# Kernel tuning notes

Hardware: AMD Instinct MI355X
Metric: run time of the kernel (lower is better)

The kernel has to match this reference:

```python
import jax, jax.numpy as jnp
import numpy as np

B, T, N, H, P = 16, 64, 512, 128, 12


def _laplacian_with_self_loop(adj):
    a = adj + jnp.eye(adj.shape[0], dtype=adj.dtype)
    d_inv_sqrt = 1.0 / jnp.sqrt(a.sum(axis=1))
    return a * d_inv_sqrt[:, None] * d_inv_sqrt[None, :]


def setup_inputs() -> dict:
    key = jax.random.key(0)
    ks = jax.random.split(key, 10)
    inputs = jax.random.normal(ks[0], (B, T, N), dtype=jnp.float32)
    adj = jax.random.uniform(ks[1], (N, N), dtype=jnp.float32)
    adj = (adj + adj.T) * 0.5
    laplacian = _laplacian_with_self_loop(adj)

    def xavier(k, shape):
        fan_in, fan_out = shape[0], shape[1]
        lim = np.sqrt(6.0 / (fan_in + fan_out))
        return jax.random.uniform(k, shape, jnp.float32, -lim, lim)

    W1 = xavier(ks[2], (H + 1, 2 * H))      # graph_conv1 weights
    b1 = jnp.ones((2 * H,), jnp.float32)    # bias init 1.0
    W2 = xavier(ks[3], (H + 1, H))          # graph_conv2 weights
    b2 = jnp.zeros((H,), jnp.float32)
    att_w1 = xavier(ks[4], (H, 1))
    att_w2 = xavier(ks[5], (N, 1))
    att_w3 = xavier(ks[6], (N, 1))
    att_b1 = jnp.zeros((1,), jnp.float32)
    att_b2 = jnp.zeros((1,), jnp.float32)
    att_b3 = jnp.zeros((1,), jnp.float32)
    W_out = xavier(ks[7], (T, P))
    b_out = jnp.zeros((P,), jnp.float32)
    return dict(inputs=inputs, laplacian=laplacian, W1=W1, b1=b1, W2=W2, b2=b2,
                att_w1=att_w1, att_w2=att_w2, att_w3=att_w3,
                att_b1=att_b1, att_b2=att_b2, att_b3=att_b3,
                W_out=W_out, b_out=b_out)


def reference(inputs, laplacian, W1, b1, W2, b2,
              att_w1, att_w2, att_w3, att_b1, att_b2, att_b3,
              W_out, b_out):
    Bs, Ts, Ns = inputs.shape
    Hs = W2.shape[1]

    def graph_conv(x_t, h_flat, W, b):
        # x_t: [B,N]; h_flat: [B, N*H]
        h = h_flat.reshape(Bs, Ns, Hs)
        conc = jnp.concatenate([x_t[..., None], h], axis=-1)     # [B,N,H+1]
        agg = jnp.einsum('mn,bnc->bmc', laplacian, conc)          # [B,N,H+1]
        out = agg @ W + b                                         # [B,N,O]
        return out.reshape(Bs, -1)                                # [B,N*O] (flattened, matching torch)

    def step(h_flat, x_t):
        ru = jax.nn.sigmoid(graph_conv(x_t, h_flat, W1, b1))      # [B, N*2H]
        r, u = jnp.split(ru, 2, axis=1)                            # split on flattened dim (faithful)
        c = jnp.tanh(graph_conv(x_t, r * h_flat, W2, b2))          # [B, N*H]
        new_h = u * h_flat + (1.0 - u) * c
        return new_h, new_h

    h0 = jnp.zeros((Bs, Ns * Hs), inputs.dtype)
    _, hs = jax.lax.scan(step, h0, jnp.moveaxis(inputs, 1, 0))     # [T,B,N*H]
    hidden_states = jnp.moveaxis(hs, 0, 1).reshape(Bs, Ts, Ns, Hs)

    # SelfAttention: project H->1, then N->1 per (b,t), softmax over T
    hs1 = hidden_states.reshape(-1, Hs) @ att_w1 + att_b1          # [B*T*N, 1]
    f = (hs1.reshape(-1, Ns) @ att_w2 + att_b2).reshape(Bs, Ts)
    g = (hs1.reshape(-1, Ns) @ att_w3 + att_b3).reshape(Bs, Ts)
    beta = jax.nn.softmax(g * f, axis=-1)                          # [B,T]
    context = beta[:, :, None] * hs1.reshape(Bs, Ts, Ns)           # [B,T,N]

    context = context.transpose(0, 2, 1)                           # [B,N,T]
    Ps = W_out.shape[1]
    out = (context.reshape(-1, Ts) @ W_out + b_out).reshape(Bs, Ns, Ps)
    return out.transpose(0, 2, 1)                                  # [B,pre_len,N]
```

## Files before the change

kernel.cpp:

```cpp
#include <hip/hip_runtime.h>
#include <math.h>

#define B_ 16
#define T_ 64
#define N_ 512
#define H_ 128
#define P_ 12
#define NH 65536

__global__ __launch_bounds__(512) void lx_kernel(const float* __restrict__ x,
                                                 const float* __restrict__ L,
                                                 float* __restrict__ Lx) {
    __shared__ __align__(16) float xs[2][N_];
    const int r0 = blockIdx.x * 2;
    const int tid = threadIdx.x;
    for (int j = 0; j < 2; ++j)
        xs[j][tid] = x[(size_t)(r0 + j) * N_ + tid];
    __syncthreads();
    float a0 = 0.f, a1 = 0.f;
    const int m = tid;
#pragma unroll 8
    for (int n = 0; n < N_; ++n) {
        float lv = L[(size_t)n * N_ + m];
        a0 += xs[0][n] * lv;
        a1 += xs[1][n] * lv;
    }
    Lx[(size_t)(r0 + 0) * N_ + m] = a0;
    Lx[(size_t)(r0 + 1) * N_ + m] = a1;
}

#define FMA4(dst, a, hv)                                                      \
    dst[0] += (a) * (hv).x; dst[1] += (a) * (hv).y;                           \
    dst[2] += (a) * (hv).z; dst[3] += (a) * (hv).w;

__global__ __launch_bounds__(512) void gc1y_kernel(
    const float* __restrict__ L, const float* __restrict__ Hprev,
    const float* __restrict__ Lx, const float* __restrict__ W1,
    const float* __restrict__ b1, const float* __restrict__ W2,
    float* __restrict__ Y, float* __restrict__ u, int t) {
    __shared__ __align__(16) union Buf {
        float Ht[2][32][H_];
        struct { float R[16][H_]; float Zb[16][H_]; } s;
    } bb;
    __shared__ __align__(16) union LW {
        float Lt[2][32][20];
        float Wt[32][260];
    } sm;

    const int tid = threadIdx.x;
    const int b = blockIdx.x & 15;
    const int mt = blockIdx.x >> 4;
    const int m0 = mt * 8;
    const float* __restrict__ Hb = Hprev + (size_t)b * NH;

    const int hrow = tid >> 5, hcol = (tid & 31) * 4;
    const int lm = tid >> 5, lk = tid & 31;
    const int lrow = (lm < 8) ? (m0 + lm) : (248 + m0 + lm);

    {
        *(float4*)&bb.Ht[0][hrow][hcol] =
            *(const float4*)&Hb[(size_t)hrow * H_ + hcol];
        *(float4*)&bb.Ht[0][hrow + 16][hcol] =
            *(const float4*)&Hb[(size_t)(hrow + 16) * H_ + hcol];
        sm.Lt[0][lk][lm] = L[(size_t)lrow * N_ + lk];
    }
    __syncthreads();

    const int g = tid >> 6;
    const int l = tid & 63;
    const int ty = l >> 4;
    const int tx = l & 15;
    const int ma0 = ty * 4;
    const int ca0 = tx * 4, cb0 = 64 + tx * 4;

    float acc[4][2][4] = {};

    for (int kc = 0; kc < 16; ++kc) {
        const int bi = kc & 1, bj = bi ^ 1;
        float4 p0, p1;
        float pl;
        if (kc < 15) {
            const size_t kb = (size_t)(kc + 1) * 32;
            p0 = *(const float4*)&Hb[(kb + hrow) * H_ + hcol];
            p1 = *(const float4*)&Hb[(kb + hrow + 16) * H_ + hcol];
            pl = L[(size_t)lrow * N_ + kb + lk];
        }
#pragma unroll
        for (int kk = 0; kk < 4; ++kk) {
            const int k = g * 4 + kk;
            const float4 la = *(const float4*)&sm.Lt[bi][k][ma0];
            const float4 h0 = *(const float4*)&bb.Ht[bi][k][ca0];
            const float4 h1 = *(const float4*)&bb.Ht[bi][k][cb0];
            FMA4(acc[0][0], la.x, h0) FMA4(acc[0][1], la.x, h1)
            FMA4(acc[1][0], la.y, h0) FMA4(acc[1][1], la.y, h1)
            FMA4(acc[2][0], la.z, h0) FMA4(acc[2][1], la.z, h1)
            FMA4(acc[3][0], la.w, h0) FMA4(acc[3][1], la.w, h1)
        }
        if (kc < 15) {
            *(float4*)&bb.Ht[bj][hrow][hcol] = p0;
            *(float4*)&bb.Ht[bj][hrow + 16][hcol] = p1;
            sm.Lt[bj][lk][lm] = pl;
        }
        __syncthreads();
    }

    for (int r = 0; r < 8; ++r) {
        if (g == r) {
#pragma unroll
            for (int i = 0; i < 4; ++i) {
#pragma unroll
                for (int v = 0; v < 2; ++v) {
                    const int c = v ? cb0 : ca0;
                    float4* zp = (float4*)&bb.s.Zb[ma0 + i][c];
                    if (r == 0) {
                        *zp = make_float4(acc[i][v][0], acc[i][v][1],
                                          acc[i][v][2], acc[i][v][3]);
                    } else {
                        float4 z = *zp;
                        *zp = make_float4(z.x + acc[i][v][0], z.y + acc[i][v][1],
                                          z.z + acc[i][v][2], z.w + acc[i][v][3]);
                    }
                }
            }
        }
        __syncthreads();
    }

    const int to = tid & 63, tm = tid >> 6;
    const int o0 = to * 4;
    float a2[2][4] = {};
    const int wr32 = tid >> 4;
    const int wcb = (tid & 15) * 16;

#pragma unroll 1
    for (int ck = 0; ck < 4; ++ck) {
#pragma unroll
        for (int q = 0; q < 4; ++q)
            *(float4*)&sm.Wt[wr32][wcb + 4 * q] =
                *(const float4*)&W1[(size_t)(1 + ck * 32 + wr32) * 256 + wcb + 4 * q];
        __syncthreads();
#pragma unroll
        for (int ch4 = 0; ch4 < 8; ++ch4) {
            const float4 w0v = *(const float4*)&sm.Wt[ch4 * 4 + 0][o0];
            const float4 w1v = *(const float4*)&sm.Wt[ch4 * 4 + 1][o0];
            const float4 w2v = *(const float4*)&sm.Wt[ch4 * 4 + 2][o0];
            const float4 w3v = *(const float4*)&sm.Wt[ch4 * 4 + 3][o0];
            const int cc = ck * 32 + ch4 * 4;
#pragma unroll
            for (int i = 0; i < 2; ++i) {
                const float4 zv = *(const float4*)&bb.s.Zb[tm + 8 * i][cc];
                a2[i][0] += zv.x * w0v.x + zv.y * w1v.x + zv.z * w2v.x + zv.w * w3v.x;
                a2[i][1] += zv.x * w0v.y + zv.y * w1v.y + zv.z * w2v.y + zv.w * w3v.y;
                a2[i][2] += zv.x * w0v.z + zv.y * w1v.z + zv.z * w2v.z + zv.w * w3v.z;
                a2[i][3] += zv.x * w0v.w + zv.y * w1v.w + zv.z * w2v.w + zv.w * w3v.w;
            }
        }
        __syncthreads();
    }

    const float4 w0r = *(const float4*)&W1[o0];
    const float4 bbv = *(const float4*)&b1[o0];
    const float* __restrict__ LxRow = Lx + ((size_t)b * T_ + t) * N_;

    {
        const float lx = LxRow[m0 + tm];
        float v0 = a2[0][0] + lx * w0r.x + bbv.x;
        float v1 = a2[0][1] + lx * w0r.y + bbv.y;
        float v2 = a2[0][2] + lx * w0r.z + bbv.z;
        float v3 = a2[0][3] + lx * w0r.w + bbv.w;
        float s0 = 1.f / (1.f + expf(-v0));
        float s1 = 1.f / (1.f + expf(-v1));
        float s2 = 1.f / (1.f + expf(-v2));
        float s3 = 1.f / (1.f + expf(-v3));
        const int fl = (m0 + tm) * 256 + o0;
        float4 hv = *(const float4*)&Hb[fl];
        const int rr2 = 2 * tm + (o0 >> 7);
        *(float4*)&bb.s.R[rr2][o0 & 127] =
            make_float4(s0 * hv.x, s1 * hv.y, s2 * hv.z, s3 * hv.w);
    }
    {
        const float lx = LxRow[256 + m0 + tm];
        float v0 = a2[1][0] + lx * w0r.x + bbv.x;
        float v1 = a2[1][1] + lx * w0r.y + bbv.y;
        float v2 = a2[1][2] + lx * w0r.z + bbv.z;
        float v3 = a2[1][3] + lx * w0r.w + bbv.w;
        float s0 = 1.f / (1.f + expf(-v0));
        float s1 = 1.f / (1.f + expf(-v1));
        float s2 = 1.f / (1.f + expf(-v2));
        float s3 = 1.f / (1.f + expf(-v3));
        float* __restrict__ uB = u + (size_t)b * NH;
        *(float4*)&uB[(m0 + tm) * 256 + o0] = make_float4(s0, s1, s2, s3);
    }
    __syncthreads();

    const int rr = tid >> 5;
    const int oc = (tid & 31) * 4;
    const int wc2 = (tid & 15) * 8;
    float a3[4] = {0.f, 0.f, 0.f, 0.f};
#pragma unroll 1
    for (int ck = 0; ck < 4; ++ck) {
        *(float4*)&sm.Wt[wr32][wc2] =
            *(const float4*)&W2[(size_t)(1 + ck * 32 + wr32) * H_ + wc2];
        *(float4*)&sm.Wt[wr32][wc2 + 4] =
            *(const float4*)&W2[(size_t)(1 + ck * 32 + wr32) * H_ + wc2 + 4];
        __syncthreads();
#pragma unroll
        for (int ch4 = 0; ch4 < 8; ++ch4) {
            const float4 w0v = *(const float4*)&sm.Wt[ch4 * 4 + 0][oc];
            const float4 w1v = *(const float4*)&sm.Wt[ch4 * 4 + 1][oc];
            const float4 w2v = *(const float4*)&sm.Wt[ch4 * 4 + 2][oc];
            const float4 w3v = *(const float4*)&sm.Wt[ch4 * 4 + 3][oc];
            const int cc = ck * 32 + ch4 * 4;
            const float4 zv = *(const float4*)&bb.s.R[rr][cc];
            a3[0] += zv.x * w0v.x + zv.y * w1v.x + zv.z * w2v.x + zv.w * w3v.x;
            a3[1] += zv.x * w0v.y + zv.y * w1v.y + zv.z * w2v.y + zv.w * w3v.y;
            a3[2] += zv.x * w0v.z + zv.y * w1v.z + zv.z * w2v.z + zv.w * w3v.z;
            a3[3] += zv.x * w0v.w + zv.y * w1v.w + zv.z * w2v.w + zv.w * w3v.w;
        }
        __syncthreads();
    }
    float* __restrict__ Yb = Y + (size_t)b * NH;
    *(float4*)&Yb[(size_t)(2 * m0 + rr) * H_ + oc] =
        make_float4(a3[0], a3[1], a3[2], a3[3]);
}

__global__ __launch_bounds__(512) void gcz_kernel(
    const float* __restrict__ L, const float* __restrict__ Y,
    const float* __restrict__ Hprev, const float* __restrict__ u,
    const float* __restrict__ Lx, const float* __restrict__ W2,
    const float* __restrict__ b2, const float* __restrict__ aw1,
    const float* __restrict__ ab1, float* __restrict__ Hnew,
    float* __restrict__ hs1, int t) {
    __shared__ __align__(16) union Buf {
        float Ht[2][32][H_];
        struct { float R[32][H_]; float Zb[16][H_]; } s;
    } bb;
    __shared__ __align__(16) float Lt[2][32][20];

    const int tid = threadIdx.x;
    const int b = blockIdx.x & 15;
    const int m0 = (blockIdx.x >> 4) * 16;
    const float* __restrict__ Yb = Y + (size_t)b * NH;

    const int hrow = tid >> 5, hcol = (tid & 31) * 4;
    const int lm = tid >> 5, lk = tid & 31;

    {
        *(float4*)&bb.Ht[0][hrow][hcol] =
            *(const float4*)&Yb[(size_t)hrow * H_ + hcol];
        *(float4*)&bb.Ht[0][hrow + 16][hcol] =
            *(const float4*)&Yb[(size_t)(hrow + 16) * H_ + hcol];
        Lt[0][lk][lm] = L[(size_t)(m0 + lm) * N_ + lk];
    }
    __syncthreads();

    const int g = tid >> 6;
    const int l = tid & 63;
    const int ty = l >> 4;
    const int tx = l & 15;
    const int ma0 = ty * 4;
    const int ca0 = tx * 4, cb0 = 64 + tx * 4;

    float acc[4][2][4] = {};

    for (int kc = 0; kc < 16; ++kc) {
        const int bi = kc & 1, bj = bi ^ 1;
        float4 p0, p1;
        float pl;
        if (kc < 15) {
            const size_t kb = (size_t)(kc + 1) * 32;
            p0 = *(const float4*)&Yb[(kb + hrow) * H_ + hcol];
            p1 = *(const float4*)&Yb[(kb + hrow + 16) * H_ + hcol];
            pl = L[(size_t)(m0 + lm) * N_ + kb + lk];
        }
#pragma unroll
        for (int kk = 0; kk < 4; ++kk) {
            const int k = g * 4 + kk;
            const float4 la = *(const float4*)&Lt[bi][k][ma0];
            const float4 h0 = *(const float4*)&bb.Ht[bi][k][ca0];
            const float4 h1 = *(const float4*)&bb.Ht[bi][k][cb0];
            FMA4(acc[0][0], la.x, h0) FMA4(acc[0][1], la.x, h1)
            FMA4(acc[1][0], la.y, h0) FMA4(acc[1][1], la.y, h1)
            FMA4(acc[2][0], la.z, h0) FMA4(acc[2][1], la.z, h1)
            FMA4(acc[3][0], la.w, h0) FMA4(acc[3][1], la.w, h1)
        }
        if (kc < 15) {
            *(float4*)&bb.Ht[bj][hrow][hcol] = p0;
            *(float4*)&bb.Ht[bj][hrow + 16][hcol] = p1;
            Lt[bj][lk][lm] = pl;
        }
        __syncthreads();
    }

    for (int r = 0; r < 8; ++r) {
        if (g == r) {
#pragma unroll
            for (int i = 0; i < 4; ++i) {
#pragma unroll
                for (int v = 0; v < 2; ++v) {
                    const int c = v ? cb0 : ca0;
                    float4* zp = (float4*)&bb.s.Zb[ma0 + i][c];
                    if (r == 0) {
                        *zp = make_float4(acc[i][v][0], acc[i][v][1],
                                          acc[i][v][2], acc[i][v][3]);
                    } else {
                        float4 z = *zp;
                        *zp = make_float4(z.x + acc[i][v][0], z.y + acc[i][v][1],
                                          z.z + acc[i][v][2], z.w + acc[i][v][3]);
                    }
                }
            }
        }
        __syncthreads();
    }

    const int zr = tid >> 5;
    const int zc = (tid & 31) * 4;
    const float4 zv = *(const float4*)&bb.s.Zb[zr][zc];
    const float4 w0r = *(const float4*)&W2[zc];
    const float4 bbv = *(const float4*)&b2[zc];
    const float4 awv = *(const float4*)&aw1[zc];
    const float lx = Lx[((size_t)b * T_ + t) * N_ + m0 + zr];

    float c0 = tanhf(zv.x + lx * w0r.x + bbv.x);
    float c1 = tanhf(zv.y + lx * w0r.y + bbv.y);
    float c2 = tanhf(zv.z + lx * w0r.z + bbv.z);
    float c3 = tanhf(zv.w + lx * w0r.w + bbv.w);

    const size_t fl = (size_t)b * NH + (size_t)(m0 + zr) * H_ + zc;
    const float4 uv = *(const float4*)&u[fl];
    const float4 hp = *(const float4*)&Hprev[fl];
    const float h0 = uv.x * hp.x + (1.f - uv.x) * c0;
    const float h1 = uv.y * hp.y + (1.f - uv.y) * c1;
    const float h2 = uv.z * hp.z + (1.f - uv.z) * c2;
    const float h3 = uv.w * hp.w + (1.f - uv.w) * c3;
    *(float4*)&Hnew[fl] = make_float4(h0, h1, h2, h3);

    float part = h0 * awv.x + h1 * awv.y + h2 * awv.z + h3 * awv.w;
#pragma unroll
    for (int off = 16; off; off >>= 1) part += __shfl_xor(part, off);
    if ((tid & 31) == 0)
        hs1[((size_t)b * T_ + t) * N_ + m0 + zr] = part + ab1[0];
}

__global__ __launch_bounds__(64) void att_beta_kernel(
    const float* __restrict__ hs1, const float* __restrict__ aw2,
    const float* __restrict__ aw3, const float* __restrict__ ab2,
    const float* __restrict__ ab3, float* __restrict__ beta) {
    const int b = blockIdx.x;
    const int t = threadIdx.x;
    const float* __restrict__ row = hs1 + ((size_t)b * T_ + t) * N_;
    float f = 0.f, g = 0.f;
    for (int n = 0; n < N_; n += 4) {
        float4 hv = *(const float4*)&row[n];
        float4 w2v = *(const float4*)&aw2[n];
        float4 w3v = *(const float4*)&aw3[n];
        f += hv.x * w2v.x + hv.y * w2v.y + hv.z * w2v.z + hv.w * w2v.w;
        g += hv.x * w3v.x + hv.y * w3v.y + hv.z * w3v.z + hv.w * w3v.w;
    }
    f += ab2[0];
    g += ab3[0];
    float s = f * g;
    float mx = s;
    for (int off = 32; off; off >>= 1) mx = fmaxf(mx, __shfl_xor(mx, off));
    float e = expf(s - mx);
    float sum = e;
    for (int off = 32; off; off >>= 1) sum += __shfl_xor(sum, off);
    beta[b * T_ + t] = e / sum;
}

__global__ __launch_bounds__(256) void att_out_kernel(
    const float* __restrict__ hs1, const float* __restrict__ beta,
    const float* __restrict__ Wout, const float* __restrict__ bout,
    float* __restrict__ out) {
    __shared__ float bs[T_];
    __shared__ float ws[T_][P_];
    const int b = blockIdx.x;
    const int tid = threadIdx.x;
    if (tid < T_) bs[tid] = beta[b * T_ + tid];
    for (int i = tid; i < T_ * P_; i += 256) ws[i / P_][i % P_] = Wout[i];
    __syncthreads();
    for (int nn = 0; nn < 2; ++nn) {
        const int n = tid + nn * 256;
        float acc[P_];
#pragma unroll
        for (int p = 0; p < P_; ++p) acc[p] = bout[p];
        for (int t = 0; t < T_; ++t) {
            float v = bs[t] * hs1[((size_t)b * T_ + t) * N_ + n];
#pragma unroll
            for (int p = 0; p < P_; ++p) acc[p] += v * ws[t][p];
        }
#pragma unroll
        for (int p = 0; p < P_; ++p) out[((size_t)b * P_ + p) * N_ + n] = acc[p];
    }
}

extern "C" void kernel_launch(void* const* d_in, const int* in_sizes, int n_in,
                              void* d_out, int out_size, void* d_ws, size_t ws_size,
                              hipStream_t stream) {
    const float* x = (const float*)d_in[0];
    const float* L = (const float*)d_in[1];
    const float* W1 = (const float*)d_in[2];
    const float* b1 = (const float*)d_in[3];
    const float* W2 = (const float*)d_in[4];
    const float* b2 = (const float*)d_in[5];
    const float* aw1 = (const float*)d_in[6];
    const float* aw2 = (const float*)d_in[7];
    const float* aw3 = (const float*)d_in[8];
    const float* ab1 = (const float*)d_in[9];
    const float* ab2 = (const float*)d_in[10];
    const float* ab3 = (const float*)d_in[11];
    const float* Wout = (const float*)d_in[12];
    const float* bout = (const float*)d_in[13];
    float* out = (float*)d_out;

    float* ws = (float*)d_ws;
    float* Lx = ws;
    float* hs1 = Lx + B_ * T_ * N_;
    float* hb0 = hs1 + B_ * T_ * N_;
    float* hb1 = hb0 + (size_t)B_ * NH;
    float* u = hb1 + (size_t)B_ * NH;
    float* Ybuf = u + (size_t)B_ * NH;
    float* beta = Ybuf + (size_t)B_ * NH;
    (void)in_sizes; (void)n_in; (void)out_size; (void)ws_size;

    hipMemsetAsync(hb0, 0, (size_t)B_ * NH * sizeof(float), stream);
    lx_kernel<<<512, 512, 0, stream>>>(x, L, Lx);

    for (int t = 0; t < T_; ++t) {
        float* hp = (t & 1) ? hb1 : hb0;
        float* hn = (t & 1) ? hb0 : hb1;
        gc1y_kernel<<<512, 512, 0, stream>>>(L, hp, Lx, W1, b1, W2, Ybuf, u, t);
        gcz_kernel<<<512, 512, 0, stream>>>(L, Ybuf, hp, u, Lx, W2, b2, aw1,
                                            ab1, hn, hs1, t);
    }
    att_beta_kernel<<<16, 64, 0, stream>>>(hs1, aw2, aw3, ab2, ab3, beta);
    att_out_kernel<<<16, 256, 0, stream>>>(hs1, beta, Wout, bout, out);
}
```

Measured before the change: 4.377 ms.

## Split graph-conv1 into an aggregation kernel and a separate gate/projection kernel

The fused gc1y kernel is split in two. gc1z computes the L·H aggregation for 16-row tiles without duplicating row pairs (m and m+256) and writes Z to global memory, reusing the hn buffer as scratch. A new ruy kernel with 1024 blocks of 256 threads loads Z rows and applies the W1 projection, the sigmoid and the W2 projection, writing r·h-derived Y or u depending on the half. This removes the duplicated L·H work per block and raises parallelism for the projection stage, at the cost of an extra launch per timestep and a global round-trip of Z.

```diff
diff --git a/kernel.cpp b/kernel.cpp
--- a/kernel.cpp
+++ b/kernel.cpp
@@ -33,36 +33,26 @@
     dst[0] += (a) * (hv).x; dst[1] += (a) * (hv).y;                           \
     dst[2] += (a) * (hv).z; dst[3] += (a) * (hv).w;
 
-__global__ __launch_bounds__(512) void gc1y_kernel(
+__global__ __launch_bounds__(512) void gc1z_kernel(
     const float* __restrict__ L, const float* __restrict__ Hprev,
-    const float* __restrict__ Lx, const float* __restrict__ W1,
-    const float* __restrict__ b1, const float* __restrict__ W2,
-    float* __restrict__ Y, float* __restrict__ u, int t) {
-    __shared__ __align__(16) union Buf {
-        float Ht[2][32][H_];
-        struct { float R[16][H_]; float Zb[16][H_]; } s;
-    } bb;
-    __shared__ __align__(16) union LW {
-        float Lt[2][32][20];
-        float Wt[32][260];
-    } sm;
+    float* __restrict__ Z) {
+    __shared__ __align__(16) float Ht[2][32][H_];
+    __shared__ __align__(16) float Lt[2][32][20];
+    __shared__ __align__(16) float Zb[16][H_];
 
     const int tid = threadIdx.x;
     const int b = blockIdx.x & 15;
-    const int mt = blockIdx.x >> 4;
-    const int m0 = mt * 8;
+    const int m0 = (blockIdx.x >> 4) * 16;
     const float* __restrict__ Hb = Hprev + (size_t)b * NH;
 
     const int hrow = tid >> 5, hcol = (tid & 31) * 4;
     const int lm = tid >> 5, lk = tid & 31;
-    const int lrow = (lm < 8) ? (m0 + lm) : (248 + m0 + lm);
 
     {
-        *(float4*)&bb.Ht[0][hrow][hcol] =
-            *(const float4*)&Hb[(size_t)hrow * H_ + hcol];
-        *(float4*)&bb.Ht[0][hrow + 16][hcol] =
+        *(float4*)&Ht[0][hrow][hcol] = *(const float4*)&Hb[(size_t)hrow * H_ + hcol];
+        *(float4*)&Ht[0][hrow + 16][hcol] =
             *(const float4*)&Hb[(size_t)(hrow + 16) * H_ + hcol];
-        sm.Lt[0][lk][lm] = L[(size_t)lrow * N_ + lk];
+        Lt[0][lk][lm] = L[(size_t)(m0 + lm) * N_ + lk];
     }
     __syncthreads();
 
@@ -83,23 +73,23 @@
             const size_t kb = (size_t)(kc + 1) * 32;
             p0 = *(const float4*)&Hb[(kb + hrow) * H_ + hcol];
             p1 = *(const float4*)&Hb[(kb + hrow + 16) * H_ + hcol];
-            pl = L[(size_t)lrow * N_ + kb + lk];
+            pl = L[(size_t)(m0 + lm) * N_ + kb + lk];
         }
 #pragma unroll
         for (int kk = 0; kk < 4; ++kk) {
             const int k = g * 4 + kk;
-            const float4 la = *(const float4*)&sm.Lt[bi][k][ma0];
-            const float4 h0 = *(const float4*)&bb.Ht[bi][k][ca0];
-            const float4 h1 = *(const float4*)&bb.Ht[bi][k][cb0];
+            const float4 la = *(const float4*)&Lt[bi][k][ma0];
+            const float4 h0 = *(const float4*)&Ht[bi][k][ca0];
+            const float4 h1 = *(const float4*)&Ht[bi][k][cb0];
             FMA4(acc[0][0], la.x, h0) FMA4(acc[0][1], la.x, h1)
             FMA4(acc[1][0], la.y, h0) FMA4(acc[1][1], la.y, h1)
             FMA4(acc[2][0], la.z, h0) FMA4(acc[2][1], la.z, h1)
             FMA4(acc[3][0], la.w, h0) FMA4(acc[3][1], la.w, h1)
         }
         if (kc < 15) {
-            *(float4*)&bb.Ht[bj][hrow][hcol] = p0;
-            *(float4*)&bb.Ht[bj][hrow + 16][hcol] = p1;
-            sm.Lt[bj][lk][lm] = pl;
+            *(float4*)&Ht[bj][hrow][hcol] = p0;
+            *(float4*)&Ht[bj][hrow + 16][hcol] = p1;
+            Lt[bj][lk][lm] = pl;
         }
         __syncthreads();
     }
@@ -111,7 +101,7 @@
 #pragma unroll
                 for (int v = 0; v < 2; ++v) {
                     const int c = v ? cb0 : ca0;
-                    float4* zp = (float4*)&bb.s.Zb[ma0 + i][c];
+                    float4* zp = (float4*)&Zb[ma0 + i][c];
                     if (r == 0) {
                         *zp = make_float4(acc[i][v][0], acc[i][v][1],
                                           acc[i][v][2], acc[i][v][3]);
@@ -126,102 +116,118 @@
         __syncthreads();
     }
 
-    const int to = tid & 63, tm = tid >> 6;
-    const int o0 = to * 4;
-    float a2[2][4] = {};
-    const int wr32 = tid >> 4;
-    const int wcb = (tid & 15) * 16;
-
+    {
+        const int zr = tid >> 5, zc = (tid & 31) * 4;
+        *(float4*)&Z[((size_t)b * NH) + (size_t)(m0 + zr) * H_ + zc] =
+            *(const float4*)&Zb[zr][zc];
+    }
+}
+
+__global__ __launch_bounds__(256) void ruy_kernel(
+    const float* __restrict__ Z, const float* __restrict__ Hprev,
+    const float* __restrict__ Lx, const float* __restrict__ W1,
+    const float* __restrict__ b1, const float* __restrict__ W2,
+    float* __restrict__ Y, float* __restrict__ u, int t) {
+    __shared__ __align__(16) float Zs[8][H_];
+    __shared__ __align__(16) float Wt[16][256];
+    __shared__ __align__(16) float Rs[16][H_];
+
+    const int tid = threadIdx.x;
+    const int b = blockIdx.x & 15;
+    const int mt = blockIdx.x >> 4;
+    const int m0 = mt * 8;
+    const int row = tid >> 5;
+    const int n = m0 + row;
+    const int o0 = (tid & 31) * 8;
+
+    {
+        const int c4 = (tid & 31) * 4;
+        *(float4*)&Zs[row][c4] =
+            *(const float4*)&Z[(size_t)b * NH + (size_t)n * H_ + c4];
+    }
+
+    float v[8] = {};
 #pragma unroll 1
-    for (int ck = 0; ck < 4; ++ck) {
-#pragma unroll
-        for (int q = 0; q < 4; ++q)
-            *(float4*)&sm.Wt[wr32][wcb + 4 * q] =
-                *(const float4*)&W1[(size_t)(1 + ck * 32 + wr32) * 256 + wcb + 4 * q];
-        __syncthreads();
-#pragma unroll
-        for (int ch4 = 0; ch4 < 8; ++ch4) {
-            const float4 w0v = *(const float4*)&sm.Wt[ch4 * 4 + 0][o0];
-            const float4 w1v = *(const float4*)&sm.Wt[ch4 * 4 + 1][o0];
-            const float4 w2v = *(const float4*)&sm.Wt[ch4 * 4 + 2][o0];
-            const float4 w3v = *(const float4*)&sm.Wt[ch4 * 4 + 3][o0];
-            const int cc = ck * 32 + ch4 * 4;
-#pragma unroll
-            for (int i = 0; i < 2; ++i) {
-                const float4 zv = *(const float4*)&bb.s.Zb[tm + 8 * i][cc];
-                a2[i][0] += zv.x * w0v.x + zv.y * w1v.x + zv.z * w2v.x + zv.w * w3v.x;
-                a2[i][1] += zv.x * w0v.y + zv.y * w1v.y + zv.z * w2v.y + zv.w * w3v.y;
-                a2[i][2] += zv.x * w0v.z + zv.y * w1v.z + zv.z * w2v.z + zv.w * w3v.z;
-                a2[i][3] += zv.x * w0v.w + zv.y * w1v.w + zv.z * w2v.w + zv.w * w3v.w;
+    for (int ck = 0; ck < 8; ++ck) {
+        __syncthreads();
+        {
+            const float4* src = (const float4*)&W1[(size_t)(1 + ck * 16) * 256];
+            float4* dst = (float4*)&Wt[0][0];
+            dst[tid] = src[tid];
+            dst[tid + 256] = src[tid + 256];
+            dst[tid + 512] = src[tid + 512];
+            dst[tid + 768] = src[tid + 768];
+        }
+        __syncthreads();
+#pragma unroll
+        for (int kk = 0; kk < 16; ++kk) {
+            const float zk = Zs[row][ck * 16 + kk];
+            const float4 wa = *(const float4*)&Wt[kk][o0];
+            const float4 wb = *(const float4*)&Wt[kk][o0 + 4];
+            v[0] += zk * wa.x; v[1] += zk * wa.y;
+            v[2] += zk * wa.z; v[3] += zk * wa.w;
+            v[4] += zk * wb.x; v[5] += zk * wb.y;
+            v[6] += zk * wb.z; v[7] += zk * wb.w;
+        }
+    }
+    __syncthreads();
+
+    const float lx = Lx[((size_t)b * T_ + t) * N_ + n];
+    float s[8];
+#pragma unroll
+    for (int j = 0; j < 8; ++j) {
+        const float vv = v[j] + lx * W1[o0 + j] + b1[o0 + j];
+        s[j] = 1.f / (1.f + expf(-vv));
+    }
+
+    if (mt < 32) {
+        const float* __restrict__ Hb = Hprev + (size_t)b * NH;
+        const int fl = n * 256 + o0;
+        const float4 h0 = *(const float4*)&Hb[fl];
+        const float4 h1 = *(const float4*)&Hb[fl + 4];
+        const int rr = 2 * row + (o0 >> 7);
+        const int rc = o0 & 127;
+        *(float4*)&Rs[rr][rc] =
+            make_float4(s[0] * h0.x, s[1] * h0.y, s[2] * h0.z, s[3] * h0.w);
+        *(float4*)&Rs[rr][rc + 4] =
+            make_float4(s[4] * h1.x, s[5] * h1.y, s[6] * h1.z, s[7] * h1.w);
+        __syncthreads();
+
+        const int yrow = tid >> 4;
+        const int yo = (tid & 15) * 8;
+        float a3[8] = {};
+#pragma unroll 1
+        for (int ck = 0; ck < 8; ++ck) {
+            {
+                const float4* src = (const float4*)&W2[(size_t)(1 + ck * 16) * H_];
+                float4* dst = (float4*)&Wt[0][0];
+                dst[tid] = src[tid];
+                dst[tid + 256] = src[tid + 256];
             }
-        }
-        __syncthreads();
-    }
-
-    const float4 w0r = *(const float4*)&W1[o0];
-    const float4 bbv = *(const float4*)&b1[o0];
-    const float* __restrict__ LxRow = Lx + ((size_t)b * T_ + t) * N_;
-
-    {
-        const float lx = LxRow[m0 + tm];
-        float v0 = a2[0][0] + lx * w0r.x + bbv.x;
-        float v1 = a2[0][1] + lx * w0r.y + bbv.y;
-        float v2 = a2[0][2] + lx * w0r.z + bbv.z;
-        float v3 = a2[0][3] + lx * w0r.w + bbv.w;
-        float s0 = 1.f / (1.f + expf(-v0));
-        float s1 = 1.f / (1.f + expf(-v1));
-        float s2 = 1.f / (1.f + expf(-v2));
-        float s3 = 1.f / (1.f + expf(-v3));
-        const int fl = (m0 + tm) * 256 + o0;
-        float4 hv = *(const float4*)&Hb[fl];
-        const int rr2 = 2 * tm + (o0 >> 7);
-        *(float4*)&bb.s.R[rr2][o0 & 127] =
-            make_float4(s0 * hv.x, s1 * hv.y, s2 * hv.z, s3 * hv.w);
-    }
-    {
-        const float lx = LxRow[256 + m0 + tm];
-        float v0 = a2[1][0] + lx * w0r.x + bbv.x;
-        float v1 = a2[1][1] + lx * w0r.y + bbv.y;
-        float v2 = a2[1][2] + lx * w0r.z + bbv.z;
-        float v3 = a2[1][3] + lx * w0r.w + bbv.w;
-        float s0 = 1.f / (1.f + expf(-v0));
-        float s1 = 1.f / (1.f + expf(-v1));
-        float s2 = 1.f / (1.f + expf(-v2));
-        float s3 = 1.f / (1.f + expf(-v3));
+            __syncthreads();
+#pragma unroll
+            for (int kk = 0; kk < 16; ++kk) {
+                const float rk = Rs[yrow][ck * 16 + kk];
+                const float* wrow = &Wt[0][0] + kk * H_;
+                const float4 wa = *(const float4*)&wrow[yo];
+                const float4 wb = *(const float4*)&wrow[yo + 4];
+                a3[0] += rk * wa.x; a3[1] += rk * wa.y;
+                a3[2] += rk * wa.z; a3[3] += rk * wa.w;
+                a3[4] += rk * wb.x; a3[5] += rk * wb.y;
+                a3[6] += rk * wb.z; a3[7] += rk * wb.w;
+            }
+            __syncthreads();
+        }
+        float* __restrict__ Yb = Y + (size_t)b * NH;
+        const size_t yoff = (size_t)(2 * m0 + yrow) * H_ + yo;
+        *(float4*)&Yb[yoff] = make_float4(a3[0], a3[1], a3[2], a3[3]);
+        *(float4*)&Yb[yoff + 4] = make_float4(a3[4], a3[5], a3[6], a3[7]);
+    } else {
         float* __restrict__ uB = u + (size_t)b * NH;
-        *(float4*)&uB[(m0 + tm) * 256 + o0] = make_float4(s0, s1, s2, s3);
-    }
-    __syncthreads();
-
-    const int rr = tid >> 5;
-    const int oc = (tid & 31) * 4;
-    const int wc2 = (tid & 15) * 8;
-    float a3[4] = {0.f, 0.f, 0.f, 0.f};
-#pragma unroll 1
-    for (int ck = 0; ck < 4; ++ck) {
-        *(float4*)&sm.Wt[wr32][wc2] =
-            *(const float4*)&W2[(size_t)(1 + ck * 32 + wr32) * H_ + wc2];
-        *(float4*)&sm.Wt[wr32][wc2 + 4] =
-            *(const float4*)&W2[(size_t)(1 + ck * 32 + wr32) * H_ + wc2 + 4];
-        __syncthreads();
-#pragma unroll
-        for (int ch4 = 0; ch4 < 8; ++ch4) {
-            const float4 w0v = *(const float4*)&sm.Wt[ch4 * 4 + 0][oc];
-            const float4 w1v = *(const float4*)&sm.Wt[ch4 * 4 + 1][oc];
-            const float4 w2v = *(const float4*)&sm.Wt[ch4 * 4 + 2][oc];
-            const float4 w3v = *(const float4*)&sm.Wt[ch4 * 4 + 3][oc];
-            const int cc = ck * 32 + ch4 * 4;
-            const float4 zv = *(const float4*)&bb.s.R[rr][cc];
-            a3[0] += zv.x * w0v.x + zv.y * w1v.x + zv.z * w2v.x + zv.w * w3v.x;
-            a3[1] += zv.x * w0v.y + zv.y * w1v.y + zv.z * w2v.y + zv.w * w3v.y;
-            a3[2] += zv.x * w0v.z + zv.y * w1v.z + zv.z * w2v.z + zv.w * w3v.z;
-            a3[3] += zv.x * w0v.w + zv.y * w1v.w + zv.z * w2v.w + zv.w * w3v.w;
-        }
-        __syncthreads();
-    }
-    float* __restrict__ Yb = Y + (size_t)b * NH;
-    *(float4*)&Yb[(size_t)(2 * m0 + rr) * H_ + oc] =
-        make_float4(a3[0], a3[1], a3[2], a3[3]);
+        const int fl = (n - 256) * 256 + o0;
+        *(float4*)&uB[fl] = make_float4(s[0], s[1], s[2], s[3]);
+        *(float4*)&uB[fl + 4] = make_float4(s[4], s[5], s[6], s[7]);
+    }
 }
 
 __global__ __launch_bounds__(512) void gcz_kernel(
@@ -430,7 +436,8 @@
     for (int t = 0; t < T_; ++t) {
         float* hp = (t & 1) ? hb1 : hb0;
         float* hn = (t & 1) ? hb0 : hb1;
-        gc1y_kernel<<<512, 512, 0, stream>>>(L, hp, Lx, W1, b1, W2, Ybuf, u, t);
+        gc1z_kernel<<<512, 512, 0, stream>>>(L, hp, hn);
+        ruy_kernel<<<1024, 256, 0, stream>>>(hn, hp, Lx, W1, b1, W2, Ybuf, u, t);
         gcz_kernel<<<512, 512, 0, stream>>>(L, Ybuf, hp, u, Lx, W2, b2, aw1,
                                             ab1, hn, hs1, t);
     }
```

Measured after the change: 5.793 ms. +32.3%, slower.
